# Performance work log

Measured on AMD Instinct MI355X. Metric: run time of the kernel, lower is better.

Reference implementation:

```python
import jax, jax.numpy as jnp
import numpy as np

B, S, L, H = 8, 4, 512, 768
N_SPANS, T_MAX = 4096, 16
N_PAIRS = 16384


def setup_inputs() -> dict:
    key = jax.random.key(0)
    k1, k2, k3, k4, k5, k6 = jax.random.split(key, 6)
    hidden = jax.random.normal(k1, (B, S, L, H), dtype=jnp.float32)
    span_doc = jax.random.randint(k2, (N_SPANS,), 0, B, dtype=jnp.int32)
    # per-span padded, sorted subtoken indices into the flattened S*L window axis
    span_tok = jnp.sort(jax.random.randint(k3, (N_SPANS, T_MAX), 0, S * L, dtype=jnp.int32), axis=1)
    span_len = jax.random.randint(k4, (N_SPANS,), 1, T_MAX + 1, dtype=jnp.int32)
    pair_i = jax.random.randint(k5, (N_PAIRS,), 0, N_SPANS, dtype=jnp.int32)
    pair_j = jax.random.randint(k6, (N_PAIRS,), 0, N_SPANS, dtype=jnp.int32)
    return {"hidden": hidden, "span_doc": span_doc, "span_tok": span_tok,
            "span_len": span_len, "pair_i": pair_i, "pair_j": pair_j}


def reference(hidden, span_doc, span_tok, span_len, pair_i, pair_j):
    # hidden: [B, S, L, H]; flatten windows so span_tok indexes S*L directly
    b, s, l, h = hidden.shape
    hf = hidden.reshape(b, s * l, h)
    # ragged gather: [N, T, H]
    g = hf[span_doc[:, None], span_tok]
    n, t = span_tok.shape
    mask = (jnp.arange(t, dtype=jnp.int32)[None, :] < span_len[:, None])  # [N, T]
    denom = span_len.astype(hidden.dtype)[:, None]
    mean = jnp.sum(g * mask[..., None].astype(hidden.dtype), axis=1) / denom  # [N, H]
    first = g[:, 0]                                      # first subtoken of span
    last = g[jnp.arange(n), span_len - 1]                # last valid subtoken
    reprs = jnp.concatenate([first, mean, last], axis=-1)  # [N, 3H]
    pairs = jnp.concatenate([reprs[pair_i], reprs[pair_j]], axis=-1)  # [P, 6H]
    return pairs
```

## Files before the change

kernel.cpp:

```cpp
#include <hip/hip_runtime.h>


#define SPAN_HF4  192
#define SPAN_TMAX 16
#define SPAN_SL   2048
#define REPR_F4   576
#define OUT_F4    1152
#define MAX_SPANS 4096

typedef float f4nt __attribute__((ext_vector_type(4)));

__device__ __forceinline__ void nt_store_f4(const float4 v, float4* p) {
    f4nt t;
    t.x = v.x; t.y = v.y; t.z = v.z; t.w = v.w;
    __builtin_nontemporal_store(t, reinterpret_cast<f4nt*>(p));
}


__global__ void zero_counts_kernel(int* __restrict__ counts, int n) {
    const int i = blockIdx.x * blockDim.x + threadIdx.x;
    if (i < n) counts[i] = 0;
}

__global__ void count_uses_kernel(const int* __restrict__ pair_i,
                                  const int* __restrict__ pair_j,
                                  int* __restrict__ counts, int n_pairs) {
    const int p = blockIdx.x * blockDim.x + threadIdx.x;
    if (p < n_pairs) {
        atomicAdd(&counts[pair_i[p]], 1);
        atomicAdd(&counts[pair_j[p]], 1);
    }
}

__global__ __launch_bounds__(1024)
void scan_offsets_kernel(const int* __restrict__ counts,
                         int* __restrict__ offsets,
                         int* __restrict__ cursor,
                         int n_spans) {
    __shared__ int sums[1024];
    const int t = threadIdx.x;
    const int base = t * 4;
    int c0 = 0, c1 = 0, c2 = 0, c3 = 0;
    if (base     < n_spans) c0 = counts[base];
    if (base + 1 < n_spans) c1 = counts[base + 1];
    if (base + 2 < n_spans) c2 = counts[base + 2];
    if (base + 3 < n_spans) c3 = counts[base + 3];
    const int local = c0 + c1 + c2 + c3;
    sums[t] = local;
    __syncthreads();
    for (int off = 1; off < 1024; off <<= 1) {
        const int v = (t >= off) ? sums[t - off] : 0;
        __syncthreads();
        sums[t] += v;
        __syncthreads();
    }
    const int excl = (t == 0) ? 0 : sums[t - 1];
    const int o0 = excl;
    const int o1 = o0 + c0;
    const int o2 = o1 + c1;
    const int o3 = o2 + c2;
    if (base     < n_spans) { offsets[base]     = o0; cursor[base]     = o0; }
    if (base + 1 < n_spans) { offsets[base + 1] = o1; cursor[base + 1] = o1; }
    if (base + 2 < n_spans) { offsets[base + 2] = o2; cursor[base + 2] = o2; }
    if (base + 3 < n_spans) { offsets[base + 3] = o3; cursor[base + 3] = o3; }
    if (t == 1023) offsets[n_spans] = sums[1023];
}

__global__ void fill_targets_kernel(const int* __restrict__ pair_i,
                                    const int* __restrict__ pair_j,
                                    int* __restrict__ cursor,
                                    int* __restrict__ targets,
                                    int n_pairs) {
    const int p = blockIdx.x * blockDim.x + threadIdx.x;
    if (p < n_pairs) {
        const int a = atomicAdd(&cursor[pair_i[p]], 1);
        targets[a] = p * 2;
        const int b = atomicAdd(&cursor[pair_j[p]], 1);
        targets[b] = p * 2 + 1;
    }
}


__global__ __launch_bounds__(192)
void span_scatter_kernel(
    const float4* __restrict__ hidden,
    const int*    __restrict__ span_doc,
    const int*    __restrict__ span_tok,
    const int*    __restrict__ span_len,
    const int*    __restrict__ offsets,
    const int*    __restrict__ targets,
    float4*       __restrict__ out)
{
    const int s = blockIdx.x;
    const int c = threadIdx.x;

    const int doc = span_doc[s];
    const int len = span_len[s];
    const int* toks = span_tok + s * SPAN_TMAX;
    const float4* base = hidden + (size_t)doc * (SPAN_SL * SPAN_HF4);

    float4 first = make_float4(0.f, 0.f, 0.f, 0.f);
    float4 last  = make_float4(0.f, 0.f, 0.f, 0.f);
    float sx = 0.f, sy = 0.f, sz = 0.f, sw = 0.f;

    #pragma unroll
    for (int t = 0; t < SPAN_TMAX; ++t) {
        const int tc = (t < len) ? t : (len - 1);
        const float4 v = base[(size_t)toks[tc] * SPAN_HF4 + c];
        if (t == 0) first = v;
        last = v;
        const float m = (t < len) ? 1.f : 0.f;
        sx += v.x * m; sy += v.y * m; sz += v.z * m; sw += v.w * m;
    }

    const float inv = 1.0f / (float)len;
    const float4 a0 = first;
    const float4 a1 = make_float4(sx * inv, sy * inv, sz * inv, sw * inv);
    const float4 a2 = last;

    __shared__ int tgt[192];
    const int start = offsets[s];
    const int end   = offsets[s + 1];
    for (int cb = start; cb < end; cb += 192) {
        const int n = min(192, end - cb);
        if (c < n) tgt[c] = targets[cb + c];
        __syncthreads();
        for (int k = 0; k < n; ++k) {
            const int tv = tgt[k];
            float4* o = out + (size_t)(tv >> 1) * OUT_F4
                            + (size_t)(tv & 1) * REPR_F4;
            nt_store_f4(a0, &o[c]);
            nt_store_f4(a1, &o[SPAN_HF4 + c]);
            nt_store_f4(a2, &o[2 * SPAN_HF4 + c]);
        }
        __syncthreads();
    }
}


__global__ __launch_bounds__(192)
void span_fused_kernel(
    const float4* __restrict__ hidden,
    const int*    __restrict__ span_doc,
    const int*    __restrict__ span_tok,
    const int*    __restrict__ span_len,
    const int*    __restrict__ pair_i,
    const int*    __restrict__ pair_j,
    float4*       __restrict__ out)
{
    const int p = blockIdx.x;
    const int c = threadIdx.x;
    const int si = pair_i[p];
    const int sj = pair_j[p];
    float4* orow = out + (size_t)p * OUT_F4;

    #pragma unroll
    for (int side = 0; side < 2; ++side) {
        const int s   = side ? sj : si;
        const int doc = span_doc[s];
        const int len = span_len[s];
        const int* toks = span_tok + s * SPAN_TMAX;
        const float4* base = hidden + (size_t)doc * (SPAN_SL * SPAN_HF4);

        float4 first = make_float4(0.f, 0.f, 0.f, 0.f);
        float4 last  = make_float4(0.f, 0.f, 0.f, 0.f);
        float sx = 0.f, sy = 0.f, sz = 0.f, sw = 0.f;
        #pragma unroll
        for (int t = 0; t < SPAN_TMAX; ++t) {
            const int tc = (t < len) ? t : (len - 1);
            const float4 v = base[(size_t)toks[tc] * SPAN_HF4 + c];
            if (t == 0) first = v;
            last = v;
            const float m = (t < len) ? 1.f : 0.f;
            sx += v.x * m; sy += v.y * m; sz += v.z * m; sw += v.w * m;
        }
        const float inv = 1.0f / (float)len;
        float4* o = orow + side * REPR_F4;
        nt_store_f4(first, &o[c]);
        nt_store_f4(make_float4(sx * inv, sy * inv, sz * inv, sw * inv),
                    &o[SPAN_HF4 + c]);
        nt_store_f4(last, &o[2 * SPAN_HF4 + c]);
    }
}


extern "C" void kernel_launch(void* const* d_in, const int* in_sizes, int n_in,
                              void* d_out, int out_size, void* d_ws, size_t ws_size,
                              hipStream_t stream) {
    const float4* hidden  = (const float4*)d_in[0];
    const int* span_doc   = (const int*)d_in[1];
    const int* span_tok   = (const int*)d_in[2];
    const int* span_len   = (const int*)d_in[3];
    const int* pair_i     = (const int*)d_in[4];
    const int* pair_j     = (const int*)d_in[5];
    float4* out           = (float4*)d_out;

    const int n_spans = in_sizes[1];
    const int n_pairs = in_sizes[4];

    auto align16 = [](size_t x) { return (x + 15) & ~(size_t)15; };
    const size_t counts_b  = align16((size_t)n_spans * sizeof(int));
    const size_t offsets_b = align16((size_t)(n_spans + 1) * sizeof(int));
    const size_t cursor_b  = align16((size_t)n_spans * sizeof(int));
    const size_t targets_b = align16((size_t)2 * n_pairs * sizeof(int));
    const size_t need = counts_b + offsets_b + cursor_b + targets_b;

    if (n_spans <= MAX_SPANS && ws_size >= need) {
        char* ws = (char*)d_ws;
        int* counts  = (int*)(ws);
        int* offsets = (int*)(ws + counts_b);
        int* cursor  = (int*)(ws + counts_b + offsets_b);
        int* targets = (int*)(ws + counts_b + offsets_b + cursor_b);

        const int zb = (n_spans + 255) / 256;
        const int pb = (n_pairs + 255) / 256;
        zero_counts_kernel<<<zb, 256, 0, stream>>>(counts, n_spans);
        count_uses_kernel<<<pb, 256, 0, stream>>>(pair_i, pair_j, counts, n_pairs);
        scan_offsets_kernel<<<1, 1024, 0, stream>>>(counts, offsets, cursor, n_spans);
        fill_targets_kernel<<<pb, 256, 0, stream>>>(pair_i, pair_j, cursor, targets, n_pairs);
        span_scatter_kernel<<<n_spans, 192, 0, stream>>>(
            hidden, span_doc, span_tok, span_len, offsets, targets, out);
    } else {
        span_fused_kernel<<<n_pairs, 192, 0, stream>>>(
            hidden, span_doc, span_tok, span_len, pair_i, pair_j, out);
    }
}
```

Before: 365.3 us.

## Split span gather and pair scatter into separate kernels via workspace reprs

Splits the fused per-span compute-and-scatter kernel into two kernels. The first writes each span's first/mean/last representation to a workspace buffer. The second reads those representations back and scatters them to every pair slot that uses the span, reading targets directly without a shared-memory staging loop or barriers. This adds a 4096x3H float round-trip through memory and an extra launch in exchange for decoupling the gather phase from the write-heavy scatter phase. It also raises the workspace requirement, so the path may fall back to the fused kernel if the workspace is too small.

```diff
diff --git a/kernel.cpp b/kernel.cpp
--- a/kernel.cpp
+++ b/kernel.cpp
@@ -82,14 +82,12 @@
 
 
 __global__ __launch_bounds__(192)
-void span_scatter_kernel(
+void span_reprs_kernel(
     const float4* __restrict__ hidden,
     const int*    __restrict__ span_doc,
     const int*    __restrict__ span_tok,
     const int*    __restrict__ span_len,
-    const int*    __restrict__ offsets,
-    const int*    __restrict__ targets,
-    float4*       __restrict__ out)
+    float4*       __restrict__ reprs)
 {
     const int s = blockIdx.x;
     const int c = threadIdx.x;
@@ -114,26 +112,38 @@
     }
 
     const float inv = 1.0f / (float)len;
-    const float4 a0 = first;
-    const float4 a1 = make_float4(sx * inv, sy * inv, sz * inv, sw * inv);
-    const float4 a2 = last;
-
-    __shared__ int tgt[192];
-    const int start = offsets[s];
-    const int end   = offsets[s + 1];
-    for (int cb = start; cb < end; cb += 192) {
-        const int n = min(192, end - cb);
-        if (c < n) tgt[c] = targets[cb + c];
-        __syncthreads();
-        for (int k = 0; k < n; ++k) {
-            const int tv = tgt[k];
+    float4* r = reprs + (size_t)s * REPR_F4;
+    r[c]                = first;
+    r[SPAN_HF4 + c]     = make_float4(sx * inv, sy * inv, sz * inv, sw * inv);
+    r[2 * SPAN_HF4 + c] = last;
+}
+
+
+__global__ __launch_bounds__(192)
+void repr_scatter_kernel(
+    const float4* __restrict__ reprs,
+    const int*    __restrict__ offsets,
+    const int*    __restrict__ targets,
+    float4*       __restrict__ out,
+    int n_spans)
+{
+    const int c = threadIdx.x;
+    for (int s = blockIdx.x; s < n_spans; s += gridDim.x) {
+        const float4* r = reprs + (size_t)s * REPR_F4;
+        const float4 a0 = r[c];
+        const float4 a1 = r[SPAN_HF4 + c];
+        const float4 a2 = r[2 * SPAN_HF4 + c];
+
+        const int start = offsets[s];
+        const int end   = offsets[s + 1];
+        for (int k = start; k < end; ++k) {
+            const int tv = targets[k];
             float4* o = out + (size_t)(tv >> 1) * OUT_F4
                             + (size_t)(tv & 1) * REPR_F4;
             nt_store_f4(a0, &o[c]);
             nt_store_f4(a1, &o[SPAN_HF4 + c]);
             nt_store_f4(a2, &o[2 * SPAN_HF4 + c]);
         }
-        __syncthreads();
     }
 }
 
@@ -203,7 +213,8 @@
     const size_t offsets_b = align16((size_t)(n_spans + 1) * sizeof(int));
     const size_t cursor_b  = align16((size_t)n_spans * sizeof(int));
     const size_t targets_b = align16((size_t)2 * n_pairs * sizeof(int));
-    const size_t need = counts_b + offsets_b + cursor_b + targets_b;
+    const size_t reprs_b   = (size_t)n_spans * REPR_F4 * sizeof(float4);
+    const size_t need = counts_b + offsets_b + cursor_b + targets_b + reprs_b;
 
     if (n_spans <= MAX_SPANS && ws_size >= need) {
         char* ws = (char*)d_ws;
@@ -211,6 +222,7 @@
         int* offsets = (int*)(ws + counts_b);
         int* cursor  = (int*)(ws + counts_b + offsets_b);
         int* targets = (int*)(ws + counts_b + offsets_b + cursor_b);
+        float4* reprs = (float4*)(ws + counts_b + offsets_b + cursor_b + targets_b);
 
         const int zb = (n_spans + 255) / 256;
         const int pb = (n_pairs + 255) / 256;
@@ -218,8 +230,10 @@
         count_uses_kernel<<<pb, 256, 0, stream>>>(pair_i, pair_j, counts, n_pairs);
         scan_offsets_kernel<<<1, 1024, 0, stream>>>(counts, offsets, cursor, n_spans);
         fill_targets_kernel<<<pb, 256, 0, stream>>>(pair_i, pair_j, cursor, targets, n_pairs);
-        span_scatter_kernel<<<n_spans, 192, 0, stream>>>(
-            hidden, span_doc, span_tok, span_len, offsets, targets, out);
+        span_reprs_kernel<<<n_spans, 192, 0, stream>>>(
+            hidden, span_doc, span_tok, span_len, reprs);
+        repr_scatter_kernel<<<n_spans, 192, 0, stream>>>(
+            reprs, offsets, targets, out, n_spans);
     } else {
         span_fused_kernel<<<n_pairs, 192, 0, stream>>>(
             hidden, span_doc, span_tok, span_len, pair_i, pair_j, out);
```

Result: slower. 376.4 us (+3.0%).

## Bucket spans by document and first-token region for cache-local gathers

Applied to the files above, without the earlier changes.

Spans are counting-sorted into buckets keyed by document and the high bits of their first token index. The scatter kernel then becomes a persistent grid with a fixed number of blocks per document, each striding through that document's bucketed span list. The intent is for concurrently running blocks to gather from the same document and nearby rows, improving L2 or MALL reuse of hidden. In exchange it adds bucket-count and bucket-fill work to the preprocessing kernels, a serial bucket scan in one thread, and load imbalance across documents.

```diff
diff --git a/kernel.cpp b/kernel.cpp
--- a/kernel.cpp
+++ b/kernel.cpp
@@ -7,6 +7,9 @@
 #define REPR_F4   576
 #define OUT_F4    1152
 #define MAX_SPANS 4096
+#define TOK_BUCKETS 16
+#define MAX_DOCS  16
+#define BPD       576
 
 typedef float f4nt __attribute__((ext_vector_type(4)));
 
@@ -17,36 +20,48 @@
 }
 
 
-__global__ void zero_counts_kernel(int* __restrict__ counts, int n) {
+__global__ void zero_kernel(int* __restrict__ pair_counts, int n_spans,
+                            int* __restrict__ bucket_counts, int nbuckets) {
     const int i = blockIdx.x * blockDim.x + threadIdx.x;
-    if (i < n) counts[i] = 0;
-}
-
-__global__ void count_uses_kernel(const int* __restrict__ pair_i,
-                                  const int* __restrict__ pair_j,
-                                  int* __restrict__ counts, int n_pairs) {
-    const int p = blockIdx.x * blockDim.x + threadIdx.x;
-    if (p < n_pairs) {
-        atomicAdd(&counts[pair_i[p]], 1);
-        atomicAdd(&counts[pair_j[p]], 1);
+    if (i < n_spans)  pair_counts[i] = 0;
+    if (i < nbuckets) bucket_counts[i] = 0;
+}
+
+__global__ void count_kernel(const int* __restrict__ pair_i,
+                             const int* __restrict__ pair_j, int n_pairs,
+                             const int* __restrict__ span_doc,
+                             const int* __restrict__ span_tok, int n_spans,
+                             int* __restrict__ pair_counts,
+                             int* __restrict__ bucket_counts) {
+    const int i = blockIdx.x * blockDim.x + threadIdx.x;
+    if (i < n_pairs) {
+        atomicAdd(&pair_counts[pair_i[i]], 1);
+        atomicAdd(&pair_counts[pair_j[i]], 1);
+    }
+    if (i < n_spans) {
+        const int b = span_doc[i] * TOK_BUCKETS + (span_tok[i * SPAN_TMAX] >> 7);
+        atomicAdd(&bucket_counts[b], 1);
     }
 }
 
 __global__ __launch_bounds__(1024)
-void scan_offsets_kernel(const int* __restrict__ counts,
-                         int* __restrict__ offsets,
-                         int* __restrict__ cursor,
-                         int n_spans) {
+void scan_kernel(const int* __restrict__ pair_counts,
+                 int* __restrict__ offsets,
+                 int* __restrict__ cursor,
+                 int n_spans,
+                 const int* __restrict__ bucket_counts,
+                 int* __restrict__ bucket_offsets,
+                 int* __restrict__ bucket_cursor,
+                 int nbuckets) {
     __shared__ int sums[1024];
     const int t = threadIdx.x;
     const int base = t * 4;
     int c0 = 0, c1 = 0, c2 = 0, c3 = 0;
-    if (base     < n_spans) c0 = counts[base];
-    if (base + 1 < n_spans) c1 = counts[base + 1];
-    if (base + 2 < n_spans) c2 = counts[base + 2];
-    if (base + 3 < n_spans) c3 = counts[base + 3];
-    const int local = c0 + c1 + c2 + c3;
-    sums[t] = local;
+    if (base     < n_spans) c0 = pair_counts[base];
+    if (base + 1 < n_spans) c1 = pair_counts[base + 1];
+    if (base + 2 < n_spans) c2 = pair_counts[base + 2];
+    if (base + 3 < n_spans) c3 = pair_counts[base + 3];
+    sums[t] = c0 + c1 + c2 + c3;
     __syncthreads();
     for (int off = 1; off < 1024; off <<= 1) {
         const int v = (t >= off) ? sums[t - off] : 0;
@@ -55,28 +70,42 @@
         __syncthreads();
     }
     const int excl = (t == 0) ? 0 : sums[t - 1];
-    const int o0 = excl;
-    const int o1 = o0 + c0;
-    const int o2 = o1 + c1;
-    const int o3 = o2 + c2;
+    const int o0 = excl, o1 = o0 + c0, o2 = o1 + c1, o3 = o2 + c2;
     if (base     < n_spans) { offsets[base]     = o0; cursor[base]     = o0; }
     if (base + 1 < n_spans) { offsets[base + 1] = o1; cursor[base + 1] = o1; }
     if (base + 2 < n_spans) { offsets[base + 2] = o2; cursor[base + 2] = o2; }
     if (base + 3 < n_spans) { offsets[base + 3] = o3; cursor[base + 3] = o3; }
     if (t == 1023) offsets[n_spans] = sums[1023];
-}
-
-__global__ void fill_targets_kernel(const int* __restrict__ pair_i,
-                                    const int* __restrict__ pair_j,
-                                    int* __restrict__ cursor,
-                                    int* __restrict__ targets,
-                                    int n_pairs) {
-    const int p = blockIdx.x * blockDim.x + threadIdx.x;
-    if (p < n_pairs) {
-        const int a = atomicAdd(&cursor[pair_i[p]], 1);
-        targets[a] = p * 2;
-        const int b = atomicAdd(&cursor[pair_j[p]], 1);
-        targets[b] = p * 2 + 1;
+    if (t == 0) {
+        int acc = 0;
+        for (int b = 0; b < nbuckets; ++b) {
+            bucket_offsets[b] = acc;
+            bucket_cursor[b]  = acc;
+            acc += bucket_counts[b];
+        }
+        bucket_offsets[nbuckets] = acc;
+    }
+}
+
+__global__ void fill_kernel(const int* __restrict__ pair_i,
+                            const int* __restrict__ pair_j, int n_pairs,
+                            const int* __restrict__ span_doc,
+                            const int* __restrict__ span_tok, int n_spans,
+                            int* __restrict__ cursor,
+                            int* __restrict__ targets,
+                            int* __restrict__ bucket_cursor,
+                            int* __restrict__ span_order) {
+    const int i = blockIdx.x * blockDim.x + threadIdx.x;
+    if (i < n_pairs) {
+        const int a = atomicAdd(&cursor[pair_i[i]], 1);
+        targets[a] = i * 2;
+        const int b = atomicAdd(&cursor[pair_j[i]], 1);
+        targets[b] = i * 2 + 1;
+    }
+    if (i < n_spans) {
+        const int b = span_doc[i] * TOK_BUCKETS + (span_tok[i * SPAN_TMAX] >> 7);
+        const int slot = atomicAdd(&bucket_cursor[b], 1);
+        span_order[slot] = i;
     }
 }
 
@@ -89,51 +118,62 @@
     const int*    __restrict__ span_len,
     const int*    __restrict__ offsets,
     const int*    __restrict__ targets,
-    float4*       __restrict__ out)
+    const int*    __restrict__ bucket_offsets,
+    const int*    __restrict__ span_order,
+    float4*       __restrict__ out,
+    int ndocs)
 {
-    const int s = blockIdx.x;
     const int c = threadIdx.x;
-
-    const int doc = span_doc[s];
-    const int len = span_len[s];
-    const int* toks = span_tok + s * SPAN_TMAX;
-    const float4* base = hidden + (size_t)doc * (SPAN_SL * SPAN_HF4);
-
-    float4 first = make_float4(0.f, 0.f, 0.f, 0.f);
-    float4 last  = make_float4(0.f, 0.f, 0.f, 0.f);
-    float sx = 0.f, sy = 0.f, sz = 0.f, sw = 0.f;
-
-    #pragma unroll
-    for (int t = 0; t < SPAN_TMAX; ++t) {
-        const int tc = (t < len) ? t : (len - 1);
-        const float4 v = base[(size_t)toks[tc] * SPAN_HF4 + c];
-        if (t == 0) first = v;
-        last = v;
-        const float m = (t < len) ? 1.f : 0.f;
-        sx += v.x * m; sy += v.y * m; sz += v.z * m; sw += v.w * m;
-    }
-
-    const float inv = 1.0f / (float)len;
-    const float4 a0 = first;
-    const float4 a1 = make_float4(sx * inv, sy * inv, sz * inv, sw * inv);
-    const float4 a2 = last;
+    const int d      = blockIdx.x % ndocs;
+    const int k0     = blockIdx.x / ndocs;
+    const int stride = gridDim.x / ndocs;
+    const int dbeg = bucket_offsets[d * TOK_BUCKETS];
+    const int dend = bucket_offsets[(d + 1) * TOK_BUCKETS];
 
     __shared__ int tgt[192];
-    const int start = offsets[s];
-    const int end   = offsets[s + 1];
-    for (int cb = start; cb < end; cb += 192) {
-        const int n = min(192, end - cb);
-        if (c < n) tgt[c] = targets[cb + c];
-        __syncthreads();
-        for (int k = 0; k < n; ++k) {
-            const int tv = tgt[k];
-            float4* o = out + (size_t)(tv >> 1) * OUT_F4
-                            + (size_t)(tv & 1) * REPR_F4;
-            nt_store_f4(a0, &o[c]);
-            nt_store_f4(a1, &o[SPAN_HF4 + c]);
-            nt_store_f4(a2, &o[2 * SPAN_HF4 + c]);
-        }
-        __syncthreads();
+
+    for (int idx = dbeg + k0; idx < dend; idx += stride) {
+        const int s = span_order[idx];
+
+        const int len = span_len[s];
+        const int* toks = span_tok + s * SPAN_TMAX;
+        const float4* base = hidden + (size_t)d * (SPAN_SL * SPAN_HF4);
+
+        float4 first = make_float4(0.f, 0.f, 0.f, 0.f);
+        float4 last  = make_float4(0.f, 0.f, 0.f, 0.f);
+        float sx = 0.f, sy = 0.f, sz = 0.f, sw = 0.f;
+
+        #pragma unroll
+        for (int t = 0; t < SPAN_TMAX; ++t) {
+            const int tc = (t < len) ? t : (len - 1);
+            const float4 v = base[(size_t)toks[tc] * SPAN_HF4 + c];
+            if (t == 0) first = v;
+            last = v;
+            const float m = (t < len) ? 1.f : 0.f;
+            sx += v.x * m; sy += v.y * m; sz += v.z * m; sw += v.w * m;
+        }
+
+        const float inv = 1.0f / (float)len;
+        const float4 a0 = first;
+        const float4 a1 = make_float4(sx * inv, sy * inv, sz * inv, sw * inv);
+        const float4 a2 = last;
+
+        const int start = offsets[s];
+        const int end   = offsets[s + 1];
+        for (int cb = start; cb < end; cb += 192) {
+            const int n = min(192, end - cb);
+            if (c < n) tgt[c] = targets[cb + c];
+            __syncthreads();
+            for (int k = 0; k < n; ++k) {
+                const int tv = tgt[k];
+                float4* o = out + (size_t)(tv >> 1) * OUT_F4
+                                + (size_t)(tv & 1) * REPR_F4;
+                nt_store_f4(a0, &o[c]);
+                nt_store_f4(a1, &o[SPAN_HF4 + c]);
+                nt_store_f4(a2, &o[2 * SPAN_HF4 + c]);
+            }
+            __syncthreads();
+        }
     }
 }
 
@@ -197,29 +237,49 @@
 
     const int n_spans = in_sizes[1];
     const int n_pairs = in_sizes[4];
+    const int ndocs   = in_sizes[0] / (SPAN_SL * 768);
 
     auto align16 = [](size_t x) { return (x + 15) & ~(size_t)15; };
-    const size_t counts_b  = align16((size_t)n_spans * sizeof(int));
-    const size_t offsets_b = align16((size_t)(n_spans + 1) * sizeof(int));
-    const size_t cursor_b  = align16((size_t)n_spans * sizeof(int));
-    const size_t targets_b = align16((size_t)2 * n_pairs * sizeof(int));
-    const size_t need = counts_b + offsets_b + cursor_b + targets_b;
-
-    if (n_spans <= MAX_SPANS && ws_size >= need) {
+    const int nbuckets = ndocs * TOK_BUCKETS;
+    const size_t pc_b  = align16((size_t)n_spans * sizeof(int));
+    const size_t off_b = align16((size_t)(n_spans + 1) * sizeof(int));
+    const size_t cur_b = align16((size_t)n_spans * sizeof(int));
+    const size_t tgt_b = align16((size_t)2 * n_pairs * sizeof(int));
+    const size_t bc_b  = align16((size_t)nbuckets * sizeof(int));
+    const size_t bo_b  = align16((size_t)(nbuckets + 1) * sizeof(int));
+    const size_t bcu_b = align16((size_t)nbuckets * sizeof(int));
+    const size_t so_b  = align16((size_t)n_spans * sizeof(int));
+    const size_t need = pc_b + off_b + cur_b + tgt_b + bc_b + bo_b + bcu_b + so_b;
+
+    if (n_spans <= MAX_SPANS && ndocs >= 1 && ndocs <= MAX_DOCS &&
+        ws_size >= need) {
         char* ws = (char*)d_ws;
-        int* counts  = (int*)(ws);
-        int* offsets = (int*)(ws + counts_b);
-        int* cursor  = (int*)(ws + counts_b + offsets_b);
-        int* targets = (int*)(ws + counts_b + offsets_b + cursor_b);
-
-        const int zb = (n_spans + 255) / 256;
-        const int pb = (n_pairs + 255) / 256;
-        zero_counts_kernel<<<zb, 256, 0, stream>>>(counts, n_spans);
-        count_uses_kernel<<<pb, 256, 0, stream>>>(pair_i, pair_j, counts, n_pairs);
-        scan_offsets_kernel<<<1, 1024, 0, stream>>>(counts, offsets, cursor, n_spans);
-        fill_targets_kernel<<<pb, 256, 0, stream>>>(pair_i, pair_j, cursor, targets, n_pairs);
-        span_scatter_kernel<<<n_spans, 192, 0, stream>>>(
-            hidden, span_doc, span_tok, span_len, offsets, targets, out);
+        int* pair_counts    = (int*)(ws);
+        int* offsets        = (int*)(ws + pc_b);
+        int* cursor         = (int*)(ws + pc_b + off_b);
+        int* targets        = (int*)(ws + pc_b + off_b + cur_b);
+        int* bucket_counts  = (int*)(ws + pc_b + off_b + cur_b + tgt_b);
+        int* bucket_offsets = (int*)(ws + pc_b + off_b + cur_b + tgt_b + bc_b);
+        int* bucket_cursor  = (int*)(ws + pc_b + off_b + cur_b + tgt_b + bc_b + bo_b);
+        int* span_order     = (int*)(ws + pc_b + off_b + cur_b + tgt_b + bc_b + bo_b + bcu_b);
+
+        const int zb = (max(n_spans, nbuckets) + 255) / 256;
+        const int cb = (max(n_pairs, n_spans) + 255) / 256;
+        zero_kernel<<<zb, 256, 0, stream>>>(pair_counts, n_spans,
+                                            bucket_counts, nbuckets);
+        count_kernel<<<cb, 256, 0, stream>>>(pair_i, pair_j, n_pairs,
+                                             span_doc, span_tok, n_spans,
+                                             pair_counts, bucket_counts);
+        scan_kernel<<<1, 1024, 0, stream>>>(pair_counts, offsets, cursor, n_spans,
+                                            bucket_counts, bucket_offsets,
+                                            bucket_cursor, nbuckets);
+        fill_kernel<<<cb, 256, 0, stream>>>(pair_i, pair_j, n_pairs,
+                                            span_doc, span_tok, n_spans,
+                                            cursor, targets,
+                                            bucket_cursor, span_order);
+        span_scatter_kernel<<<ndocs * BPD, 192, 0, stream>>>(
+            hidden, span_doc, span_tok, span_len,
+            offsets, targets, bucket_offsets, span_order, out, ndocs);
     } else {
         span_fused_kernel<<<n_pairs, 192, 0, stream>>>(
             hidden, span_doc, span_tok, span_len, pair_i, pair_j, out);
```

Result: slower. 381.7 us (+4.5%).
